# Kernel tuning notes

Measured on AMD Instinct MI355X. Metric: run time of the kernel, lower is better.

Reference implementation:

```python
import jax, jax.numpy as jnp
import numpy as np

N = 50000   # nodes
E = 400000  # edges
B = 50      # graphs in the batch
DIMS = [32, 8, 16, 64, 256, 512]  # in_channels, then hidden*{1,2,8,32,64}


def setup_inputs() -> dict:
    key = jax.random.key(0)
    ks = jax.random.split(key, 16)
    inp = {
        "x": jax.random.normal(ks[0], (N, DIMS[0]), dtype=jnp.float32),
        "edge_index": jax.random.randint(ks[1], (2, E), 0, N, dtype=jnp.int64),
        "batch": jnp.sort(jax.random.randint(ks[2], (N,), 0, B, dtype=jnp.int64)),
    }
    for i in range(5):
        fan_in, fan_out = DIMS[i], DIMS[i + 1]
        scale = jnp.float32(1.0 / np.sqrt(fan_in))  # glorot-ish
        inp[f"W{i+1}"] = jax.random.normal(ks[3 + 2 * i], (fan_in, fan_out), dtype=jnp.float32) * scale
        inp[f"b{i+1}"] = jnp.zeros((fan_out,), dtype=jnp.float32)
    return inp


def _gcn_conv(x, W, b, src, dst, edge_norm, self_norm):
    # PyG GCNConv: h = x @ W, then propagate over A_hat = D^-1/2 (A + I) D^-1/2, then + bias
    h = x @ W                                                  # [N, out]
    msg = h[src] * edge_norm[:, None]                          # gather + scale, [E, out]
    agg = jax.ops.segment_sum(msg, dst, num_segments=N)        # scatter-add, [N, out]
    return agg + h * self_norm[:, None] + b                    # self-loop term = h_i / deg_i


def reference(x, edge_index, batch, W1, b1, W2, b2, W3, b3, W4, b4, W5, b5):
    src, dst = edge_index[0], edge_index[1]
    # degree with self-loops (PyG computes deg on the col/dst index)
    deg = jax.ops.segment_sum(jnp.ones((E,), x.dtype), dst, num_segments=N) + 1.0
    dinv = jax.lax.rsqrt(deg)                                  # deg^-1/2
    edge_norm = dinv[src] * dinv[dst]                          # [E]
    self_norm = dinv * dinv                                    # 1/deg, [N]

    for W, b in ((W1, b1), (W2, b2), (W3, b3), (W4, b4), (W5, b5)):
        x = jax.nn.relu(_gcn_conv(x, W, b, src, dst, edge_norm, self_norm))

    # global_mean_pool over graph ids
    counts = jax.ops.segment_sum(jnp.ones((N,), x.dtype), batch, num_segments=B)
    sums = jax.ops.segment_sum(x, batch, num_segments=B)       # [B, 512]
    return sums / jnp.maximum(counts, 1.0)[:, None]
```

## Files before the change

### kernel.cpp

```cpp
#include <hip/hip_runtime.h>
#include <hip/hip_bf16.h>

#define NNODES 50000
#define NEDGES 400000
#define NGRAPH 50

typedef __bf16 bf16_t;
typedef __bf16 bf16x4_t __attribute__((ext_vector_type(4)));
typedef __bf16 bf16x8_t __attribute__((ext_vector_type(8)));
typedef float f32x4_t __attribute__((ext_vector_type(4)));


__global__ void count_kernel(const int* __restrict__ dst, int* __restrict__ cnt, int E) {
    int e = blockIdx.x * 256 + threadIdx.x;
    if (e < E) atomicAdd(&cnt[dst[e]], 1);
}

__global__ void dinv_kernel(const int* __restrict__ cnt, float* __restrict__ dinv, int N) {
    int i = blockIdx.x * 256 + threadIdx.x;
    if (i < N) dinv[i] = rsqrtf((float)cnt[i] + 1.0f);
}

__global__ void scan_part(const int* __restrict__ cnt, int* __restrict__ bsum,
                          int* __restrict__ pre, int N) {
    __shared__ int sm[256];
    int t = threadIdx.x;
    int i = blockIdx.x * 256 + t;
    sm[t] = (i < N) ? cnt[i] : 0;
    __syncthreads();
    for (int off = 1; off < 256; off <<= 1) {
        int x = (t >= off) ? sm[t - off] : 0;
        __syncthreads();
        sm[t] += x;
        __syncthreads();
    }
    if (i < N) pre[i] = sm[t];
    if (t == 255) bsum[blockIdx.x] = sm[255];
}

__global__ void scan_bsum(int* __restrict__ bsum, int nb) {
    __shared__ int sm[256];
    int t = threadIdx.x;
    sm[t] = (t < nb) ? bsum[t] : 0;
    __syncthreads();
    for (int off = 1; off < 256; off <<= 1) {
        int x = (t >= off) ? sm[t - off] : 0;
        __syncthreads();
        sm[t] += x;
        __syncthreads();
    }
    if (t < nb) bsum[t] = sm[t];
}

__global__ void scan_final(const int* __restrict__ pre, const int* __restrict__ bsum,
                           int* __restrict__ row_ptr, int N) {
    int i = blockIdx.x * 256 + threadIdx.x;
    if (i == 0) row_ptr[0] = 0;
    if (i < N) {
        int off = (blockIdx.x > 0) ? bsum[blockIdx.x - 1] : 0;
        row_ptr[i + 1] = off + pre[i];
    }
}

__global__ void fill_kernel(const int* __restrict__ src, const int* __restrict__ dst,
                            const int* __restrict__ row_ptr, int* __restrict__ fill,
                            const float* __restrict__ dinv,
                            int* __restrict__ col, float* __restrict__ ew, int E) {
    int e = blockIdx.x * 256 + threadIdx.x;
    if (e < E) {
        int s = src[e], d = dst[e];
        int pos = row_ptr[d] + atomicAdd(&fill[d], 1);
        col[pos] = s;
        ew[pos] = dinv[s] * dinv[d];
    }
}

__global__ void graph_starts(const int* __restrict__ batch, int* __restrict__ start, int N) {
    int i = blockIdx.x * 256 + threadIdx.x;
    if (i >= N) return;
    int b = batch[i];
    if (i == 0) {
        for (int g = 0; g <= b; ++g) start[g] = 0;
    } else {
        int p = batch[i - 1];
        for (int g = p + 1; g <= b; ++g) start[g] = i;
    }
    if (i == N - 1) {
        for (int g = b + 1; g <= NGRAPH; ++g) start[g] = N;
    }
}

template <int K, int C>
__global__ void prep_w_packed(const float* __restrict__ W, bf16_t* __restrict__ hi,
                              bf16_t* __restrict__ lo) {
    constexpr int KT = K / 32;
    int i = blockIdx.x * 256 + threadIdx.x;
    if (i < K * C) {
        int j = i & 7;
        int lane = (i >> 3) & 63;
        int rest = i >> 9;
        int kc8 = rest % KT;
        int cb = rest / KT;
        int k = kc8 * 32 + ((lane >> 4) << 3) + j;
        int c = cb * 16 + (lane & 15);
        float v = W[k * C + c];
        bf16_t h = (bf16_t)v;
        float r = v - (float)h;
        hi[i] = h;
        lo[i] = (bf16_t)r;
    }
}


template <int CIN, int COUT, int RPT, bool PR, typename InT = float, typename OutT = float>
__global__ __launch_bounds__(256) void transform_persist(const InT* __restrict__ X,
                                                         const float* __restrict__ W,
                                                         const float* __restrict__ bias,
                                                         OutT* __restrict__ Y, int N) {
    constexpr int RT = RPT * COUT / 256;
    __shared__ float Ws[CIN * COUT];
    __shared__ float ps[RPT * CIN];
    int t = threadIdx.x;
    for (int i = t; i < CIN * COUT; i += 256) Ws[i] = W[i];

    int j = t % COUT;
    int lb = (t / COUT) * RT;
    float bv = 0.f;
    if constexpr (PR) bv = bias[j];

    int ntiles = (N + RPT - 1) / RPT;
    for (int tile = blockIdx.x; tile < ntiles; tile += gridDim.x) {
        int row0 = tile * RPT;
        __syncthreads();
        for (int i = t; i < RPT * CIN; i += 256) {
            int r = row0 + i / CIN;
            ps[i] = (r < N) ? (float)X[r * CIN + (i % CIN)] : 0.f;
        }
        __syncthreads();

        float acc[RT];
        #pragma unroll
        for (int r = 0; r < RT; ++r) acc[r] = bv;
        #pragma unroll
        for (int k = 0; k < CIN; ++k) {
            float w = Ws[k * COUT + j];
            #pragma unroll
            for (int r = 0; r < RT; ++r) acc[r] += ps[(lb + r) * CIN + k] * w;
        }
        #pragma unroll
        for (int r = 0; r < RT; ++r) {
            int row = row0 + lb + r;
            if (row < N) {
                float v = acc[r];
                if constexpr (PR) v = fmaxf(v, 0.f);
                Y[row * COUT + j] = (OutT)v;
            }
        }
    }
}


template <int C, bool PR, typename InT = float, typename OutT = float>
__global__ void propagate_kernel(const InT* __restrict__ xin, OutT* __restrict__ xout,
                                 const int* __restrict__ row_ptr, const int* __restrict__ col,
                                 const float* __restrict__ ew, const float* __restrict__ dinv,
                                 const float* __restrict__ bias, int N) {
    constexpr int NPB = 256 / C;
    int t = threadIdx.x;
    int node = blockIdx.x * NPB + t / C;
    int ch = t % C;
    if (node >= N) return;
    float di = dinv[node];
    float acc = (float)xin[node * C + ch] * di * di;
    int e0 = row_ptr[node], e1 = row_ptr[node + 1];
    for (int e = e0; e < e1; ++e) {
        acc += (float)xin[col[e] * C + ch] * ew[e];
    }
    if constexpr (PR) acc = fmaxf(acc + bias[ch], 0.f);
    xout[node * C + ch] = (OutT)acc;
}


__global__ __launch_bounds__(256) void propagate256_bf16(
    const bf16_t* __restrict__ xin, bf16_t* __restrict__ xout,
    const int* __restrict__ row_ptr, const int* __restrict__ col,
    const float* __restrict__ ew, const float* __restrict__ dinv, int N)
{
    int t = threadIdx.x;
    int node = blockIdx.x * 4 + (t >> 6);
    if (node >= N) return;
    int lane = t & 63;
    size_t base = (size_t)node * 256 + lane * 4;
    float di = dinv[node];
    float sn = di * di;
    bf16x4_t sv = *reinterpret_cast<const bf16x4_t*>(&xin[base]);
    float a0 = (float)sv[0] * sn, a1 = (float)sv[1] * sn;
    float a2 = (float)sv[2] * sn, a3 = (float)sv[3] * sn;
    int e0 = row_ptr[node], e1 = row_ptr[node + 1];
    for (int e = e0; e < e1; ++e) {
        int s = col[e];
        float w = ew[e];
        bf16x4_t v = *reinterpret_cast<const bf16x4_t*>(&xin[(size_t)s * 256 + lane * 4]);
        a0 += w * (float)v[0]; a1 += w * (float)v[1];
        a2 += w * (float)v[2]; a3 += w * (float)v[3];
    }
    bf16x4_t o;
    o[0] = (bf16_t)a0; o[1] = (bf16_t)a1; o[2] = (bf16_t)a2; o[3] = (bf16_t)a3;
    *reinterpret_cast<bf16x4_t*>(&xout[base]) = o;
}


__global__ __launch_bounds__(256) void transform4_mfma(
    const bf16_t* __restrict__ A, const bf16_t* __restrict__ Wth,
    const bf16_t* __restrict__ Wtl, const float* __restrict__ bias,
    bf16_t* __restrict__ Y, int N)
{
    __shared__ bf16_t As[64 * 64];
    int t = threadIdx.x;
    int wave = t >> 6, lane = t & 63;
    int wr = wave >> 1, wc = wave & 1;
    int lr = lane & 15, kg = lane >> 4;
    int brow = blockIdx.x * 64;

    #pragma unroll
    for (int i = 0; i < 2; ++i) {
        int idx = i * 256 + t;
        int row = idx >> 3, kq = idx & 7;
        int gr = brow + row; if (gr > N - 1) gr = N - 1;
        bf16x8_t v = *reinterpret_cast<const bf16x8_t*>(&A[(size_t)gr * 64 + kq * 8]);
        *reinterpret_cast<bf16x8_t*>(&As[row * 64 + ((kq ^ (row & 7)) << 3)]) = v;
    }
    __syncthreads();

    int r0l = wr * 32 + lr;
    int r1l = r0l + 16;

    #pragma unroll
    for (int ct = 0; ct < 2; ++ct) {
        int colw = ct * 128 + wc * 64;
        int cbbase = colw >> 4;
        f32x4_t acc[2][4];
        #pragma unroll
        for (int i = 0; i < 2; ++i)
            #pragma unroll
            for (int j = 0; j < 4; ++j) {
                f32x4_t z = {0.f, 0.f, 0.f, 0.f};
                acc[i][j] = z;
            }

        #pragma unroll
        for (int kc8 = 0; kc8 < 2; ++kc8) {
            int kq = kc8 * 4 + kg;
            bf16x8_t a0 = *reinterpret_cast<const bf16x8_t*>(&As[r0l * 64 + ((kq ^ (r0l & 7)) << 3)]);
            bf16x8_t a1 = *reinterpret_cast<const bf16x8_t*>(&As[r1l * 64 + ((kq ^ (r1l & 7)) << 3)]);
            #pragma unroll
            for (int cf = 0; cf < 4; ++cf) {
                int cb = cbbase + cf;
                size_t bo = (((size_t)(cb * 2 + kc8)) << 9) + (lane << 3);
                bf16x8_t bh = *reinterpret_cast<const bf16x8_t*>(&Wth[bo]);
                bf16x8_t bl = *reinterpret_cast<const bf16x8_t*>(&Wtl[bo]);
                acc[0][cf] = __builtin_amdgcn_mfma_f32_16x16x32_bf16(a0, bh, acc[0][cf], 0, 0, 0);
                acc[0][cf] = __builtin_amdgcn_mfma_f32_16x16x32_bf16(a0, bl, acc[0][cf], 0, 0, 0);
                acc[1][cf] = __builtin_amdgcn_mfma_f32_16x16x32_bf16(a1, bh, acc[1][cf], 0, 0, 0);
                acc[1][cf] = __builtin_amdgcn_mfma_f32_16x16x32_bf16(a1, bl, acc[1][cf], 0, 0, 0);
            }
        }

        #pragma unroll
        for (int cf = 0; cf < 4; ++cf) {
            float bv = bias[colw + cf * 16 + lr];
            #pragma unroll
            for (int rf = 0; rf < 2; ++rf)
                #pragma unroll
                for (int g = 0; g < 4; ++g) {
                    int r = brow + wr * 32 + rf * 16 + kg * 4 + g;
                    if (r < N)
                        Y[(size_t)r * 256 + colw + cf * 16 + lr] =
                            (bf16_t)fmaxf(acc[rf][cf][g] + bv, 0.f);
                }
        }
    }
}


__global__ __launch_bounds__(256) void gemm5_pool_mfma(
    const bf16_t* __restrict__ A, const bf16_t* __restrict__ Wth,
    const bf16_t* __restrict__ Wtl, const float* __restrict__ bias,
    const int* __restrict__ batch, float* __restrict__ out, int N)
{
    __shared__ bf16_t As[64 * 256];
    __shared__ float red[512];
    int t = threadIdx.x;
    int wave = t >> 6, lane = t & 63;
    int wr = wave >> 1, wc = wave & 1;
    int lr = lane & 15, kg = lane >> 4;
    int brow = blockIdx.x * 64;

    #pragma unroll
    for (int i = 0; i < 8; ++i) {
        int idx = i * 256 + t;
        int row = idx >> 5, kq = idx & 31;
        int gr = brow + row; if (gr > N - 1) gr = N - 1;
        bf16x8_t v = *reinterpret_cast<const bf16x8_t*>(&A[(size_t)gr * 256 + kq * 8]);
        *reinterpret_cast<bf16x8_t*>(&As[row * 256 + ((kq ^ (row & 7)) << 3)]) = v;
    }
    red[t] = 0.f;
    red[t + 256] = 0.f;
    __syncthreads();

    int rlast = brow + 63; if (rlast > N - 1) rlast = N - 1;
    bool uniform = (batch[brow] == batch[rlast]);
    int r0l = wr * 32 + lr;
    int r1l = r0l + 16;

    int bb[2][4];
    if (!uniform) {
        #pragma unroll
        for (int rf = 0; rf < 2; ++rf)
            #pragma unroll
            for (int g = 0; g < 4; ++g) {
                int r = brow + wr * 32 + rf * 16 + kg * 4 + g;
                bb[rf][g] = (r < N) ? batch[r] : -1;
            }
    }

    for (int ct = 0; ct < 4; ++ct) {
        int colw = ct * 128 + wc * 64;
        int cbbase = colw >> 4;
        f32x4_t acc[2][4];
        #pragma unroll
        for (int i = 0; i < 2; ++i)
            #pragma unroll
            for (int j = 0; j < 4; ++j) {
                f32x4_t z = {0.f, 0.f, 0.f, 0.f};
                acc[i][j] = z;
            }

        #pragma unroll
        for (int kc8 = 0; kc8 < 8; ++kc8) {
            int kq = kc8 * 4 + kg;
            bf16x8_t a0 = *reinterpret_cast<const bf16x8_t*>(&As[r0l * 256 + ((kq ^ (r0l & 7)) << 3)]);
            bf16x8_t a1 = *reinterpret_cast<const bf16x8_t*>(&As[r1l * 256 + ((kq ^ (r1l & 7)) << 3)]);
            #pragma unroll
            for (int cf = 0; cf < 4; ++cf) {
                int cb = cbbase + cf;
                size_t bo = (((size_t)(cb * 8 + kc8)) << 9) + (lane << 3);
                bf16x8_t bh = *reinterpret_cast<const bf16x8_t*>(&Wth[bo]);
                bf16x8_t bl = *reinterpret_cast<const bf16x8_t*>(&Wtl[bo]);
                acc[0][cf] = __builtin_amdgcn_mfma_f32_16x16x32_bf16(a0, bh, acc[0][cf], 0, 0, 0);
                acc[0][cf] = __builtin_amdgcn_mfma_f32_16x16x32_bf16(a0, bl, acc[0][cf], 0, 0, 0);
                acc[1][cf] = __builtin_amdgcn_mfma_f32_16x16x32_bf16(a1, bh, acc[1][cf], 0, 0, 0);
                acc[1][cf] = __builtin_amdgcn_mfma_f32_16x16x32_bf16(a1, bl, acc[1][cf], 0, 0, 0);
            }
        }

        #pragma unroll
        for (int cf = 0; cf < 4; ++cf) {
            float bv = bias[colw + cf * 16 + lr];
            if (uniform) {
                float s = 0.f;
                #pragma unroll
                for (int rf = 0; rf < 2; ++rf)
                    #pragma unroll
                    for (int g = 0; g < 4; ++g) {
                        int r = brow + wr * 32 + rf * 16 + kg * 4 + g;
                        float vv = fmaxf(acc[rf][cf][g] + bv, 0.f);
                        s += (r < N) ? vv : 0.f;
                    }
                s += __shfl_xor(s, 16, 64);
                s += __shfl_xor(s, 32, 64);
                if (lane < 16) atomicAdd(&red[colw + cf * 16 + lr], s);
            } else {
                #pragma unroll
                for (int rf = 0; rf < 2; ++rf)
                    #pragma unroll
                    for (int g = 0; g < 4; ++g) {
                        float vv = fmaxf(acc[rf][cf][g] + bv, 0.f);
                        if (bb[rf][g] >= 0)
                            atomicAdd(&out[(size_t)bb[rf][g] * 512 + colw + cf * 16 + lr], vv);
                    }
            }
        }
    }

    if (uniform) {
        __syncthreads();
        int b0 = batch[brow];
        atomicAdd(&out[(size_t)b0 * 512 + t], red[t]);
        atomicAdd(&out[(size_t)b0 * 512 + t + 256], red[t + 256]);
    }
}

__global__ void divide_kernel(float* __restrict__ out, const int* __restrict__ start, int total) {
    int i = blockIdx.x * 256 + threadIdx.x;
    if (i < total) {
        int g = i >> 9;
        float c = (float)(start[g + 1] - start[g]);
        out[i] /= fmaxf(c, 1.f);
    }
}


extern "C" void kernel_launch(void* const* d_in, const int* in_sizes, int n_in,
                              void* d_out, int out_size, void* d_ws, size_t ws_size,
                              hipStream_t stream) {
    const float* x   = (const float*)d_in[0];
    const int* ei    = (const int*)d_in[1];
    const int* batch = (const int*)d_in[2];
    const float* W1 = (const float*)d_in[3];  const float* b1 = (const float*)d_in[4];
    const float* W2 = (const float*)d_in[5];  const float* b2 = (const float*)d_in[6];
    const float* W3 = (const float*)d_in[7];  const float* b3 = (const float*)d_in[8];
    const float* W4 = (const float*)d_in[9];  const float* b4 = (const float*)d_in[10];
    const float* W5 = (const float*)d_in[11]; const float* b5 = (const float*)d_in[12];
    float* out = (float*)d_out;

    const int N = NNODES, E = NEDGES;
    const int* src = ei;
    const int* dst = ei + E;

    char* ws = (char*)d_ws;
    size_t off = 0;
    auto alloc = [&](size_t bytes) {
        void* p = ws + off;
        off += (bytes + 255) & ~size_t(255);
        return p;
    };
    float* bufA   = (float*)alloc(sizeof(float) * size_t(N) * 256);
    float* bufB   = (float*)alloc(sizeof(float) * size_t(N) * 256);
    int* cnt      = (int*)alloc(sizeof(int) * N);
    int* fill     = (int*)alloc(sizeof(int) * N);
    int* row_ptr  = (int*)alloc(sizeof(int) * (N + 1));
    int* col      = (int*)alloc(sizeof(int) * E);
    float* ew     = (float*)alloc(sizeof(float) * E);
    float* dinv   = (float*)alloc(sizeof(float) * N);
    int* gstart   = (int*)alloc(sizeof(int) * (NGRAPH + 1));
    int* pre      = (int*)alloc(sizeof(int) * N);
    int* bsum     = (int*)alloc(sizeof(int) * 256);
    bf16_t* wt_hi = (bf16_t*)alloc(sizeof(bf16_t) * 512 * 256);
    bf16_t* wt_lo = (bf16_t*)alloc(sizeof(bf16_t) * 512 * 256);
    bf16_t* w4_hi = (bf16_t*)alloc(sizeof(bf16_t) * 256 * 64);
    bf16_t* w4_lo = (bf16_t*)alloc(sizeof(bf16_t) * 256 * 64);

    hipMemsetAsync(cnt, 0, sizeof(int) * N, stream);
    hipMemsetAsync(fill, 0, sizeof(int) * N, stream);
    hipMemsetAsync(out, 0, sizeof(float) * out_size, stream);

    count_kernel<<<(E + 255) / 256, 256, 0, stream>>>(dst, cnt, E);
    dinv_kernel<<<(N + 255) / 256, 256, 0, stream>>>(cnt, dinv, N);
    int nb = (N + 255) / 256;
    scan_part<<<nb, 256, 0, stream>>>(cnt, bsum, pre, N);
    scan_bsum<<<1, 256, 0, stream>>>(bsum, nb);
    scan_final<<<nb, 256, 0, stream>>>(pre, bsum, row_ptr, N);
    fill_kernel<<<(E + 255) / 256, 256, 0, stream>>>(src, dst, row_ptr, fill, dinv, col, ew, E);
    graph_starts<<<nb, 256, 0, stream>>>(batch, gstart, N);
    prep_w_packed<256, 512><<<(256 * 512 + 255) / 256, 256, 0, stream>>>(W5, wt_hi, wt_lo);
    prep_w_packed<64, 256><<<(64 * 256 + 255) / 256, 256, 0, stream>>>(W4, w4_hi, w4_lo);

    transform_persist<32, 8, 32, false><<<1024, 256, 0, stream>>>(x, W1, nullptr, bufA, N);
    propagate_kernel<8, true><<<(N + 31) / 32, 256, 0, stream>>>(bufA, bufB, row_ptr, col, ew, dinv, b1, N);

    propagate_kernel<8, false><<<(N + 31) / 32, 256, 0, stream>>>(bufB, bufA, row_ptr, col, ew, dinv, nullptr, N);
    transform_persist<8, 16, 32, true><<<1024, 256, 0, stream>>>(bufA, W2, b2, bufB, N);

    propagate_kernel<16, false><<<(N + 15) / 16, 256, 0, stream>>>(bufB, bufA, row_ptr, col, ew, dinv, nullptr, N);
    bf16_t* h3b = (bf16_t*)bufB;
    transform_persist<16, 64, 16, true, float, bf16_t><<<1024, 256, 0, stream>>>(bufA, W3, b3, h3b, N);

    bf16_t* h4a = (bf16_t*)bufA;
    propagate_kernel<64, false, bf16_t, bf16_t><<<(N + 3) / 4, 256, 0, stream>>>(h3b, h4a, row_ptr, col, ew, dinv, nullptr, N);
    bf16_t* h4b = (bf16_t*)bufB;
    transform4_mfma<<<(N + 63) / 64, 256, 0, stream>>>(h4a, w4_hi, w4_lo, b4, h4b, N);

    bf16_t* h5in = (bf16_t*)bufA;
    propagate256_bf16<<<(N + 3) / 4, 256, 0, stream>>>(h4b, h5in, row_ptr, col, ew, dinv, N);
    gemm5_pool_mfma<<<(N + 63) / 64, 256, 0, stream>>>(h5in, wt_hi, wt_lo, b5, batch, out, N);
    divide_kernel<<<(NGRAPH * 512 + 255) / 256, 256, 0, stream>>>(out, gstart, NGRAPH * 512);
}
```

Before: 417.8 us.

## Fuse dinv into scan_final and retile MFMA GEMMs for full-row waves

The separate dinv kernel launch is removed and rsqrt of the degree is computed inside scan_final. In both MFMA GEMM kernels each wave now covers all 64 rows and a 64-column strip, in place of a 2x2 wave grid over 32-row halves. Each B fragment is therefore reused across four row fragments, which cuts weight loads, at the cost of more accumulator registers. The pooling kernel drops the LDS atomics and zero-init of red, writing each column slot directly because each column is now owned by exactly one wave.

After: 414.9 us. Within noise of the previous version (-0.7%).

```diff
diff --git a/kernel.cpp b/kernel.cpp
--- a/kernel.cpp
+++ b/kernel.cpp
@@ -14,11 +14,6 @@
 __global__ void count_kernel(const int* __restrict__ dst, int* __restrict__ cnt, int E) {
     int e = blockIdx.x * 256 + threadIdx.x;
     if (e < E) atomicAdd(&cnt[dst[e]], 1);
-}
-
-__global__ void dinv_kernel(const int* __restrict__ cnt, float* __restrict__ dinv, int N) {
-    int i = blockIdx.x * 256 + threadIdx.x;
-    if (i < N) dinv[i] = rsqrtf((float)cnt[i] + 1.0f);
 }
 
 __global__ void scan_part(const int* __restrict__ cnt, int* __restrict__ bsum,
@@ -53,12 +48,14 @@
 }
 
 __global__ void scan_final(const int* __restrict__ pre, const int* __restrict__ bsum,
-                           int* __restrict__ row_ptr, int N) {
+                           const int* __restrict__ cnt,
+                           int* __restrict__ row_ptr, float* __restrict__ dinv, int N) {
     int i = blockIdx.x * 256 + threadIdx.x;
     if (i == 0) row_ptr[0] = 0;
     if (i < N) {
         int off = (blockIdx.x > 0) ? bsum[blockIdx.x - 1] : 0;
         row_ptr[i + 1] = off + pre[i];
+        dinv[i] = rsqrtf((float)cnt[i] + 1.0f);
     }
 }
 
@@ -218,7 +215,6 @@
     __shared__ bf16_t As[64 * 64];
     int t = threadIdx.x;
     int wave = t >> 6, lane = t & 63;
-    int wr = wave >> 1, wc = wave & 1;
     int lr = lane & 15, kg = lane >> 4;
     int brow = blockIdx.x * 64;
 
@@ -232,53 +228,52 @@
     }
     __syncthreads();
 
-    int r0l = wr * 32 + lr;
-    int r1l = r0l + 16;
-
-    #pragma unroll
-    for (int ct = 0; ct < 2; ++ct) {
-        int colw = ct * 128 + wc * 64;
-        int cbbase = colw >> 4;
-        f32x4_t acc[2][4];
-        #pragma unroll
-        for (int i = 0; i < 2; ++i)
-            #pragma unroll
-            for (int j = 0; j < 4; ++j) {
-                f32x4_t z = {0.f, 0.f, 0.f, 0.f};
-                acc[i][j] = z;
-            }
-
-        #pragma unroll
-        for (int kc8 = 0; kc8 < 2; ++kc8) {
-            int kq = kc8 * 4 + kg;
-            bf16x8_t a0 = *reinterpret_cast<const bf16x8_t*>(&As[r0l * 64 + ((kq ^ (r0l & 7)) << 3)]);
-            bf16x8_t a1 = *reinterpret_cast<const bf16x8_t*>(&As[r1l * 64 + ((kq ^ (r1l & 7)) << 3)]);
-            #pragma unroll
-            for (int cf = 0; cf < 4; ++cf) {
-                int cb = cbbase + cf;
-                size_t bo = (((size_t)(cb * 2 + kc8)) << 9) + (lane << 3);
-                bf16x8_t bh = *reinterpret_cast<const bf16x8_t*>(&Wth[bo]);
-                bf16x8_t bl = *reinterpret_cast<const bf16x8_t*>(&Wtl[bo]);
-                acc[0][cf] = __builtin_amdgcn_mfma_f32_16x16x32_bf16(a0, bh, acc[0][cf], 0, 0, 0);
-                acc[0][cf] = __builtin_amdgcn_mfma_f32_16x16x32_bf16(a0, bl, acc[0][cf], 0, 0, 0);
-                acc[1][cf] = __builtin_amdgcn_mfma_f32_16x16x32_bf16(a1, bh, acc[1][cf], 0, 0, 0);
-                acc[1][cf] = __builtin_amdgcn_mfma_f32_16x16x32_bf16(a1, bl, acc[1][cf], 0, 0, 0);
-            }
-        }
-
+    int colw = wave * 64;
+    int cbbase = colw >> 4;
+    f32x4_t acc[4][4];
+    #pragma unroll
+    for (int i = 0; i < 4; ++i)
+        #pragma unroll
+        for (int j = 0; j < 4; ++j) {
+            f32x4_t z = {0.f, 0.f, 0.f, 0.f};
+            acc[i][j] = z;
+        }
+
+    #pragma unroll
+    for (int kc8 = 0; kc8 < 2; ++kc8) {
+        int kq = kc8 * 4 + kg;
+        bf16x8_t a[4];
+        #pragma unroll
+        for (int rf = 0; rf < 4; ++rf) {
+            int rl = rf * 16 + lr;
+            a[rf] = *reinterpret_cast<const bf16x8_t*>(&As[rl * 64 + ((kq ^ (rl & 7)) << 3)]);
+        }
         #pragma unroll
         for (int cf = 0; cf < 4; ++cf) {
-            float bv = bias[colw + cf * 16 + lr];
-            #pragma unroll
-            for (int rf = 0; rf < 2; ++rf)
-                #pragma unroll
-                for (int g = 0; g < 4; ++g) {
-                    int r = brow + wr * 32 + rf * 16 + kg * 4 + g;
-                    if (r < N)
-                        Y[(size_t)r * 256 + colw + cf * 16 + lr] =
-                            (bf16_t)fmaxf(acc[rf][cf][g] + bv, 0.f);
-                }
-        }
+            int cb = cbbase + cf;
+            size_t bo = (((size_t)(cb * 2 + kc8)) << 9) + (lane << 3);
+            bf16x8_t bh = *reinterpret_cast<const bf16x8_t*>(&Wth[bo]);
+            bf16x8_t bl = *reinterpret_cast<const bf16x8_t*>(&Wtl[bo]);
+            #pragma unroll
+            for (int rf = 0; rf < 4; ++rf) {
+                acc[rf][cf] = __builtin_amdgcn_mfma_f32_16x16x32_bf16(a[rf], bh, acc[rf][cf], 0, 0, 0);
+                acc[rf][cf] = __builtin_amdgcn_mfma_f32_16x16x32_bf16(a[rf], bl, acc[rf][cf], 0, 0, 0);
+            }
+        }
+    }
+
+    #pragma unroll
+    for (int cf = 0; cf < 4; ++cf) {
+        float bv = bias[colw + cf * 16 + lr];
+        #pragma unroll
+        for (int rf = 0; rf < 4; ++rf)
+            #pragma unroll
+            for (int g = 0; g < 4; ++g) {
+                int r = brow + rf * 16 + kg * 4 + g;
+                if (r < N)
+                    Y[(size_t)r * 256 + colw + cf * 16 + lr] =
+                        (bf16_t)fmaxf(acc[rf][cf][g] + bv, 0.f);
+            }
     }
 }
 
@@ -292,7 +287,6 @@
     __shared__ float red[512];
     int t = threadIdx.x;
     int wave = t >> 6, lane = t & 63;
-    int wr = wave >> 1, wc = wave & 1;
     int lr = lane & 15, kg = lane >> 4;
     int brow = blockIdx.x * 64;
 
@@ -304,32 +298,29 @@
         bf16x8_t v = *reinterpret_cast<const bf16x8_t*>(&A[(size_t)gr * 256 + kq * 8]);
         *reinterpret_cast<bf16x8_t*>(&As[row * 256 + ((kq ^ (row & 7)) << 3)]) = v;
     }
-    red[t] = 0.f;
-    red[t + 256] = 0.f;
     __syncthreads();
 
     int rlast = brow + 63; if (rlast > N - 1) rlast = N - 1;
     bool uniform = (batch[brow] == batch[rlast]);
-    int r0l = wr * 32 + lr;
-    int r1l = r0l + 16;
-
-    int bb[2][4];
+
+    int bb[4][4];
     if (!uniform) {
         #pragma unroll
-        for (int rf = 0; rf < 2; ++rf)
+        for (int rf = 0; rf < 4; ++rf)
             #pragma unroll
             for (int g = 0; g < 4; ++g) {
-                int r = brow + wr * 32 + rf * 16 + kg * 4 + g;
+                int r = brow + rf * 16 + kg * 4 + g;
                 bb[rf][g] = (r < N) ? batch[r] : -1;
             }
     }
 
-    for (int ct = 0; ct < 4; ++ct) {
-        int colw = ct * 128 + wc * 64;
+    #pragma unroll
+    for (int ct = 0; ct < 2; ++ct) {
+        int colw = ct * 256 + wave * 64;
         int cbbase = colw >> 4;
-        f32x4_t acc[2][4];
-        #pragma unroll
-        for (int i = 0; i < 2; ++i)
+        f32x4_t acc[4][4];
+        #pragma unroll
+        for (int i = 0; i < 4; ++i)
             #pragma unroll
             for (int j = 0; j < 4; ++j) {
                 f32x4_t z = {0.f, 0.f, 0.f, 0.f};
@@ -339,18 +330,23 @@
         #pragma unroll
         for (int kc8 = 0; kc8 < 8; ++kc8) {
             int kq = kc8 * 4 + kg;
-            bf16x8_t a0 = *reinterpret_cast<const bf16x8_t*>(&As[r0l * 256 + ((kq ^ (r0l & 7)) << 3)]);
-            bf16x8_t a1 = *reinterpret_cast<const bf16x8_t*>(&As[r1l * 256 + ((kq ^ (r1l & 7)) << 3)]);
+            bf16x8_t a[4];
+            #pragma unroll
+            for (int rf = 0; rf < 4; ++rf) {
+                int rl = rf * 16 + lr;
+                a[rf] = *reinterpret_cast<const bf16x8_t*>(&As[rl * 256 + ((kq ^ (rl & 7)) << 3)]);
+            }
             #pragma unroll
             for (int cf = 0; cf < 4; ++cf) {
                 int cb = cbbase + cf;
                 size_t bo = (((size_t)(cb * 8 + kc8)) << 9) + (lane << 3);
                 bf16x8_t bh = *reinterpret_cast<const bf16x8_t*>(&Wth[bo]);
                 bf16x8_t bl = *reinterpret_cast<const bf16x8_t*>(&Wtl[bo]);
-                acc[0][cf] = __builtin_amdgcn_mfma_f32_16x16x32_bf16(a0, bh, acc[0][cf], 0, 0, 0);
-                acc[0][cf] = __builtin_amdgcn_mfma_f32_16x16x32_bf16(a0, bl, acc[0][cf], 0, 0, 0);
-                acc[1][cf] = __builtin_amdgcn_mfma_f32_16x16x32_bf16(a1, bh, acc[1][cf], 0, 0, 0);
-                acc[1][cf] = __builtin_amdgcn_mfma_f32_16x16x32_bf16(a1, bl, acc[1][cf], 0, 0, 0);
+                #pragma unroll
+                for (int rf = 0; rf < 4; ++rf) {
+                    acc[rf][cf] = __builtin_amdgcn_mfma_f32_16x16x32_bf16(a[rf], bh, acc[rf][cf], 0, 0, 0);
+                    acc[rf][cf] = __builtin_amdgcn_mfma_f32_16x16x32_bf16(a[rf], bl, acc[rf][cf], 0, 0, 0);
+                }
             }
         }
 
@@ -360,19 +356,19 @@
             if (uniform) {
                 float s = 0.f;
                 #pragma unroll
-                for (int rf = 0; rf < 2; ++rf)
+                for (int rf = 0; rf < 4; ++rf)
                     #pragma unroll
                     for (int g = 0; g < 4; ++g) {
-                        int r = brow + wr * 32 + rf * 16 + kg * 4 + g;
+                        int r = brow + rf * 16 + kg * 4 + g;
                         float vv = fmaxf(acc[rf][cf][g] + bv, 0.f);
                         s += (r < N) ? vv : 0.f;
                     }
                 s += __shfl_xor(s, 16, 64);
                 s += __shfl_xor(s, 32, 64);
-                if (lane < 16) atomicAdd(&red[colw + cf * 16 + lr], s);
+                if (lane < 16) red[colw + cf * 16 + lr] = s;
             } else {
                 #pragma unroll
-                for (int rf = 0; rf < 2; ++rf)
+                for (int rf = 0; rf < 4; ++rf)
                     #pragma unroll
                     for (int g = 0; g < 4; ++g) {
                         float vv = fmaxf(acc[rf][cf][g] + bv, 0.f);
@@ -446,11 +442,10 @@
     hipMemsetAsync(out, 0, sizeof(float) * out_size, stream);
 
     count_kernel<<<(E + 255) / 256, 256, 0, stream>>>(dst, cnt, E);
-    dinv_kernel<<<(N + 255) / 256, 256, 0, stream>>>(cnt, dinv, N);
     int nb = (N + 255) / 256;
     scan_part<<<nb, 256, 0, stream>>>(cnt, bsum, pre, N);
     scan_bsum<<<1, 256, 0, stream>>>(bsum, nb);
-    scan_final<<<nb, 256, 0, stream>>>(pre, bsum, row_ptr, N);
+    scan_final<<<nb, 256, 0, stream>>>(pre, bsum, cnt, row_ptr, dinv, N);
     fill_kernel<<<(E + 255) / 256, 256, 0, stream>>>(src, dst, row_ptr, fill, dinv, col, ew, E);
     graph_starts<<<nb, 256, 0, stream>>>(batch, gstart, N);
     prep_w_packed<256, 512><<<(256 * 512 + 255) / 256, 256, 0, stream>>>(W5, wt_hi, wt_lo);
```
